# Kernel optimization log

Hardware: AMD Instinct MI355X
Metric: run time of the kernel (lower is better)

The kernel has to match this reference:

```python
import jax, jax.numpy as jnp
import numpy as np

D_MODEL, NHEAD, INT_DIM = 1024, 16, 4096
HEAD_DIM = D_MODEL // NHEAD
EPS = 1e-5


def _layernorm(x, gamma, beta):
    mu = jnp.mean(x, axis=-1, keepdims=True)
    var = jnp.var(x, axis=-1, keepdims=True)
    return (x - mu) * jax.lax.rsqrt(var + EPS) * gamma + beta


def setup_inputs() -> dict:
    key = jax.random.key(0)
    ks = jax.random.split(key, 16)
    B, T = 2, 2048
    s = 0.02
    inp = {
        'x': jax.random.normal(ks[0], (B, T, D_MODEL), dtype=jnp.float32),
        'Wq': jax.random.normal(ks[1], (D_MODEL, D_MODEL), dtype=jnp.float32) * s,
        'bq': jnp.zeros((D_MODEL,), jnp.float32),
        'Wk': jax.random.normal(ks[2], (D_MODEL, D_MODEL), dtype=jnp.float32) * s,
        'bk': jnp.zeros((D_MODEL,), jnp.float32),
        'Wv': jax.random.normal(ks[3], (D_MODEL, D_MODEL), dtype=jnp.float32) * s,
        'bv': jnp.zeros((D_MODEL,), jnp.float32),
        'Wo': jax.random.normal(ks[4], (D_MODEL, D_MODEL), dtype=jnp.float32) * s,
        'bo': jnp.zeros((D_MODEL,), jnp.float32),
        'ln1_g': jnp.ones((D_MODEL,), jnp.float32),
        'ln1_b': jnp.zeros((D_MODEL,), jnp.float32),
        'ln2_g': jnp.ones((D_MODEL,), jnp.float32),
        'ln2_b': jnp.zeros((D_MODEL,), jnp.float32),
        'W1': jax.random.normal(ks[5], (D_MODEL, INT_DIM), dtype=jnp.float32) * s,
        'b1': jnp.zeros((INT_DIM,), jnp.float32),
        'W2': jax.random.normal(ks[6], (INT_DIM, D_MODEL), dtype=jnp.float32) * s,
        'b2': jnp.zeros((D_MODEL,), jnp.float32),
    }
    return inp


def reference(x, Wq, bq, Wk, bk, Wv, bv, Wo, bo, ln1_g, ln1_b, ln2_g, ln2_b, W1, b1, W2, b2):
    B, T, D = x.shape
    # projections
    q = (x @ Wq + bq).reshape(B, T, NHEAD, HEAD_DIM).transpose(0, 2, 1, 3)
    k = (x @ Wk + bk).reshape(B, T, NHEAD, HEAD_DIM).transpose(0, 2, 1, 3)
    v = (x @ Wv + bv).reshape(B, T, NHEAD, HEAD_DIM).transpose(0, 2, 1, 3)
    # attention: [B,H,T,T] scores, softmax over keys
    scores = jnp.einsum('bhqd,bhkd->bhqk', q, k) / jnp.sqrt(jnp.float32(HEAD_DIM))
    attn = jax.nn.softmax(scores, axis=-1)
    out = jnp.einsum('bhqk,bhkd->bhqd', attn, v)
    out = out.transpose(0, 2, 1, 3).reshape(B, T, D)
    attn_output = out @ Wo + bo
    # residual + layernorm 1
    h = _layernorm(x + attn_output, ln1_g, ln1_b)
    # FFN
    ff = jax.nn.relu(h @ W1 + b1) @ W2 + b2
    # residual + layernorm 2
    return _layernorm(h + ff, ln2_g, ln2_b)
```

## Files before the change

### kernel.cpp

```cpp
#include <hip/hip_runtime.h>
#include <cstdint>

#define DEVI __device__ __forceinline__

typedef float f32x4 __attribute__((ext_vector_type(4)));
typedef __bf16 bf16x8 __attribute__((ext_vector_type(8)));
typedef unsigned int u32x4v __attribute__((ext_vector_type(4)));
typedef unsigned short u16;
typedef unsigned int u32;
typedef unsigned long long u64;

#define LOG2E 1.44269504088896f
#define QSCALE (0.125f * LOG2E)

DEVI u16 bf16bits(float f) {
    u32 u = __builtin_bit_cast(u32, f);
    u32 r = u + 0x7fffu + ((u >> 16) & 1u);
    return (u16)(r >> 16);
}

DEVI u32 pack2bf(float a, float b) {
    u16 x = __builtin_bit_cast(u16, (__bf16)a);
    u16 y = __builtin_bit_cast(u16, (__bf16)b);
    return (u32)x | ((u32)y << 16);
}

DEVI void gload16(const void* g, const void* l) {
    __builtin_amdgcn_global_load_lds(
        (const __attribute__((address_space(1))) void*)(u64)(uintptr_t)g,
        (__attribute__((address_space(3))) void*)(u32)(uintptr_t)l,
        16, 0, 0);
}

#define VMCNT0_BARRIER()                                   \
    asm volatile("s_waitcnt vmcnt(0)" ::: "memory");       \
    __builtin_amdgcn_s_barrier()

__global__ __launch_bounds__(256)
void prep_kernel(const float* __restrict__ x, u16* __restrict__ xb,
                 const float* __restrict__ Wq, const float* __restrict__ Wk,
                 const float* __restrict__ Wv, const float* __restrict__ Wo,
                 u16* __restrict__ Wqt, u16* __restrict__ Wkt,
                 u16* __restrict__ Wvt, u16* __restrict__ Wot,
                 const float* __restrict__ W1, u16* __restrict__ W1t,
                 const float* __restrict__ W2, u16* __restrict__ W2t) {
    __shared__ float t[64][65];
    const int b = blockIdx.x;
    const int tid = threadIdx.x;
    if (b < 4096) {
        int i = b * 256 + tid;
        float4 v = ((const float4*)x)[i];
        ((uint2*)xb)[i] = make_uint2(pack2bf(v.x, v.y), pack2bf(v.z, v.w));
        return;
    }
    const float* src;
    u16* dst;
    int K_, N_, k0, n0;
    if (b < 5120) {
        int l = b - 4096;
        int z = l >> 8;
        l &= 255;
        src = z == 0 ? Wq : z == 1 ? Wk : z == 2 ? Wv : Wo;
        dst = z == 0 ? Wqt : z == 1 ? Wkt : z == 2 ? Wvt : Wot;
        K_ = 1024; N_ = 1024;
        k0 = (l & 15) * 64; n0 = (l >> 4) * 64;
    } else if (b < 6144) {
        int l = b - 5120;
        src = W1; dst = W1t; K_ = 1024; N_ = 4096;
        k0 = (l & 15) * 64; n0 = (l >> 4) * 64;
    } else {
        int l = b - 6144;
        src = W2; dst = W2t; K_ = 4096; N_ = 1024;
        k0 = (l & 63) * 64; n0 = (l >> 6) * 64;
    }
#pragma unroll
    for (int i = 0; i < 16; i++) {
        int idx = i * 256 + tid;
        int r = idx >> 6, c = idx & 63;
        t[r][c] = src[(u64)(k0 + r) * N_ + n0 + c];
    }
    __syncthreads();
#pragma unroll
    for (int i = 0; i < 16; i++) {
        int idx = i * 256 + tid;
        int r = idx >> 6, c = idx & 63;
        dst[(u64)(n0 + r) * K_ + k0 + c] = bf16bits(t[c][r]);
    }
}

enum { MODE_QK = 0, MODE_VT = 1, MODE_RESID = 2, MODE_RELU = 3 };

DEVI void gemm_core(const u16* __restrict__ A, const u16* __restrict__ Bt, int K_,
                    u16 (*ldsA)[128 * 64], u16 (*ldsB)[128 * 64],
                    f32x4 (&acc)[4][4], int m0, int n0) {
    const int tid = threadIdx.x;
    const int lane = tid & 63;
    const int wid = tid >> 6;
    const int wr = wid >> 1, wc = wid & 1;
    const int l15 = lane & 15, l4 = lane >> 4;
    const int srow = tid >> 3;
    const int sc = (tid & 7) ^ (srow & 7);

    const u16* ap[4];
    const u16* bp[4];
#pragma unroll
    for (int i = 0; i < 4; i++) {
        ap[i] = A + (u64)(m0 + i * 32 + srow) * K_ + sc * 8;
        bp[i] = Bt + (u64)(n0 + i * 32 + srow) * K_ + sc * 8;
    }

    auto stage = [&](int buf) {
#pragma unroll
        for (int i = 0; i < 4; i++) {
            gload16(ap[i], (const char*)ldsA[buf] + (i * 256 + tid) * 16);
            ap[i] += 64;
        }
#pragma unroll
        for (int i = 0; i < 4; i++) {
            gload16(bp[i], (const char*)ldsB[buf] + (i * 256 + tid) * 16);
            bp[i] += 64;
        }
    };

    auto compute = [&](const u16* A_, const u16* B_) {
#pragma unroll
        for (int ks = 0; ks < 2; ks++) {
            bf16x8 af[4], bfr[4];
#pragma unroll
            for (int mi = 0; mi < 4; mi++) {
                int row = wr * 64 + mi * 16 + l15;
                af[mi] = *(const bf16x8*)((const char*)A_ + row * 128 +
                                          (((ks * 4 + l4) ^ (row & 7)) * 16));
            }
#pragma unroll
            for (int ni = 0; ni < 4; ni++) {
                int row = wc * 64 + ni * 16 + l15;
                bfr[ni] = *(const bf16x8*)((const char*)B_ + row * 128 +
                                           (((ks * 4 + l4) ^ (row & 7)) * 16));
            }
            __builtin_amdgcn_s_setprio(1);
#pragma unroll
            for (int mi = 0; mi < 4; mi++)
#pragma unroll
                for (int ni = 0; ni < 4; ni++)
                    acc[mi][ni] = __builtin_amdgcn_mfma_f32_16x16x32_bf16(
                        af[mi], bfr[ni], acc[mi][ni], 0, 0, 0);
            __builtin_amdgcn_s_setprio(0);
        }
    };

    const int nk = K_ >> 6;
    stage(0);
    VMCNT0_BARRIER();
    for (int t = 0; t < nk; t += 2) {
        if (t + 1 < nk) stage(1);
        compute(ldsA[0], ldsB[0]);
        VMCNT0_BARRIER();
        if (t + 2 < nk) stage(0);
        compute(ldsA[1], ldsB[1]);
        VMCNT0_BARRIER();
    }
}

template <int MODE>
DEVI void gemm_epilogue(f32x4 (&acc)[4][4], const float* __restrict__ bias,
                        const float* __restrict__ resid, void* __restrict__ outp,
                        int N_, int m0, int n0, float scale) {
    const int tid = threadIdx.x;
    const int lane = tid & 63;
    const int wid = tid >> 6;
    const int wr = wid >> 1, wc = wid & 1;
    const int l15 = lane & 15, l4 = lane >> 4;
#pragma unroll
    for (int mi = 0; mi < 4; mi++) {
#pragma unroll
        for (int ni = 0; ni < 4; ni++) {
            const int n = n0 + wc * 64 + ni * 16 + l15;
            const float bv = bias[n];
            const int mb = m0 + wr * 64 + mi * 16 + l4 * 4;
            if (MODE == MODE_VT) {
                const int b = mb >> 11, t = mb & 2047;
                const int hh = n >> 6, d = n & 63;
                u32 lo = pack2bf(acc[mi][ni][0] + bv, acc[mi][ni][1] + bv);
                u32 hi = pack2bf(acc[mi][ni][2] + bv, acc[mi][ni][3] + bv);
                u64 idx = ((u64)((b << 4) + hh) * 64 + d) * 2048 + t;
                *(uint2*)((u16*)outp + idx) = make_uint2(lo, hi);
            } else {
#pragma unroll
                for (int r = 0; r < 4; r++) {
                    const int m = mb + r;
                    const float v = acc[mi][ni][r] + bv;
                    if (MODE == MODE_QK) {
                        const int b = m >> 11, t = m & 2047;
                        const int hh = n >> 6, d = n & 63;
                        ((u16*)outp)[(((u64)((b << 4) + hh) * 2048 + t) << 6) + d] =
                            bf16bits(v * scale);
                    } else if (MODE == MODE_RESID) {
                        const u64 i2 = (u64)m * N_ + n;
                        ((float*)outp)[i2] = v + resid[i2];
                    } else {
                        ((u16*)outp)[(u64)m * N_ + n] = bf16bits(fmaxf(v, 0.f));
                    }
                }
            }
        }
    }
}

template <int MODE>
__global__ __launch_bounds__(256, 2)
void gemm_kernel(const u16* __restrict__ A, const u16* __restrict__ Bt,
                 const float* __restrict__ bias, const float* __restrict__ resid,
                 void* __restrict__ outp, int N_, int K_) {
    __shared__ u16 ldsA[2][128 * 64];
    __shared__ u16 ldsB[2][128 * 64];
    const int m0 = blockIdx.x * 128;
    const int n0 = blockIdx.y * 128;
    f32x4 acc[4][4];
#pragma unroll
    for (int i = 0; i < 4; i++)
#pragma unroll
        for (int j = 0; j < 4; j++) acc[i][j] = (f32x4){0.f, 0.f, 0.f, 0.f};
    gemm_core(A, Bt, K_, ldsA, ldsB, acc, m0, n0);
    gemm_epilogue<MODE>(acc, bias, resid, outp, N_, m0, n0, 1.f);
}

__global__ __launch_bounds__(256, 2)
void gemm_qkv_kernel(const u16* __restrict__ A,
                     const u16* __restrict__ Wq, const u16* __restrict__ Wk,
                     const u16* __restrict__ Wv,
                     const float* __restrict__ bq, const float* __restrict__ bk,
                     const float* __restrict__ bv,
                     u16* __restrict__ Qo, u16* __restrict__ Ko, u16* __restrict__ Vo) {
    __shared__ u16 ldsA[2][128 * 64];
    __shared__ u16 ldsB[2][128 * 64];
    const int z = blockIdx.z;
    const u16* Bt = z == 0 ? Wq : z == 1 ? Wk : Wv;
    const float* bias = z == 0 ? bq : z == 1 ? bk : bv;
    const int m0 = blockIdx.x * 128;
    const int n0 = blockIdx.y * 128;
    f32x4 acc[4][4];
#pragma unroll
    for (int i = 0; i < 4; i++)
#pragma unroll
        for (int j = 0; j < 4; j++) acc[i][j] = (f32x4){0.f, 0.f, 0.f, 0.f};
    gemm_core(A, Bt, 1024, ldsA, ldsB, acc, m0, n0);
    if (z == 2)
        gemm_epilogue<MODE_VT>(acc, bias, nullptr, Vo, 1024, m0, n0, 1.f);
    else
        gemm_epilogue<MODE_QK>(acc, bias, nullptr, z == 0 ? Qo : Ko, 1024, m0, n0,
                               z == 0 ? QSCALE : 1.f);
}

__global__ __launch_bounds__(256, 2)
void gemm_n64_kernel(const u16* __restrict__ A, const u16* __restrict__ Bt,
                     const float* __restrict__ bias, const float* __restrict__ resid,
                     float* __restrict__ outp, int K_) {
    __shared__ u16 ldsA[2][128 * 64];
    __shared__ u16 ldsB[2][64 * 64];
    const int tid = threadIdx.x;
    const int lane = tid & 63;
    const int wid = tid >> 6;
    const int m0 = blockIdx.x * 128;
    const int n0 = blockIdx.y * 64;
    const int l15 = lane & 15, l4 = lane >> 4;
    const int srow = tid >> 3;
    const int sc = (tid & 7) ^ (srow & 7);

    const u16* ap[4];
    const u16* bp[2];
#pragma unroll
    for (int i = 0; i < 4; i++)
        ap[i] = A + (u64)(m0 + i * 32 + srow) * K_ + sc * 8;
#pragma unroll
    for (int i = 0; i < 2; i++)
        bp[i] = Bt + (u64)(n0 + i * 32 + srow) * K_ + sc * 8;

    auto stage = [&](int buf) {
#pragma unroll
        for (int i = 0; i < 4; i++) {
            gload16(ap[i], (const char*)ldsA[buf] + (i * 256 + tid) * 16);
            ap[i] += 64;
        }
#pragma unroll
        for (int i = 0; i < 2; i++) {
            gload16(bp[i], (const char*)ldsB[buf] + (i * 256 + tid) * 16);
            bp[i] += 64;
        }
    };

    f32x4 acc[2][4];
#pragma unroll
    for (int i = 0; i < 2; i++)
#pragma unroll
        for (int j = 0; j < 4; j++) acc[i][j] = (f32x4){0.f, 0.f, 0.f, 0.f};

    auto compute = [&](const u16* A_, const u16* B_) {
#pragma unroll
        for (int ks = 0; ks < 2; ks++) {
            bf16x8 af[2], bfr[4];
#pragma unroll
            for (int mi = 0; mi < 2; mi++) {
                int row = wid * 32 + mi * 16 + l15;
                af[mi] = *(const bf16x8*)((const char*)A_ + row * 128 +
                                          (((ks * 4 + l4) ^ (row & 7)) * 16));
            }
#pragma unroll
            for (int ni = 0; ni < 4; ni++) {
                int row = ni * 16 + l15;
                bfr[ni] = *(const bf16x8*)((const char*)B_ + row * 128 +
                                           (((ks * 4 + l4) ^ (row & 7)) * 16));
            }
            __builtin_amdgcn_s_setprio(1);
#pragma unroll
            for (int mi = 0; mi < 2; mi++)
#pragma unroll
                for (int ni = 0; ni < 4; ni++)
                    acc[mi][ni] = __builtin_amdgcn_mfma_f32_16x16x32_bf16(
                        af[mi], bfr[ni], acc[mi][ni], 0, 0, 0);
            __builtin_amdgcn_s_setprio(0);
        }
    };

    const int nk = K_ >> 6;
    stage(0);
    VMCNT0_BARRIER();
    for (int t = 0; t < nk; t += 2) {
        if (t + 1 < nk) stage(1);
        compute(ldsA[0], ldsB[0]);
        VMCNT0_BARRIER();
        if (t + 2 < nk) stage(0);
        compute(ldsA[1], ldsB[1]);
        VMCNT0_BARRIER();
    }

#pragma unroll
    for (int mi = 0; mi < 2; mi++) {
#pragma unroll
        for (int ni = 0; ni < 4; ni++) {
            const int n = n0 + ni * 16 + l15;
            const float bv = bias[n];
            const int mb = m0 + wid * 32 + mi * 16 + l4 * 4;
#pragma unroll
            for (int r = 0; r < 4; r++) {
                const u64 i2 = (u64)(mb + r) * 1024 + n;
                outp[i2] = acc[mi][ni][r] + bv + resid[i2];
            }
        }
    }
}

__global__ __launch_bounds__(256, 5)
void attn_kernel(const u16* __restrict__ Qg, const u16* __restrict__ Kg,
                 const u16* __restrict__ Vtg, u16* __restrict__ Og) {
    __shared__ u16 ldsK[2][64 * 64];
    __shared__ u16 ldsV[2][64 * 64];
    const int tid = threadIdx.x;
    const int lane = tid & 63;
    const int w = tid >> 6;
    const int l15 = lane & 15, l4 = lane >> 4;
    const int id = blockIdx.x;
    const int swz = (id & 7) * 128 + (id >> 3);
    const int bh = swz >> 5;
    const int qblk = swz & 31;
    const u64 kvbase = (u64)bh * 2048 * 64;
    const int qw0 = qblk * 64 + w * 16;

    const int srow = tid >> 3;
    const int sc8 = ((tid & 7) ^ (srow & 7)) * 8;
    const u16* kq0 = Kg + kvbase + (u64)srow * 64 + sc8;
    const u16* kq1 = Kg + kvbase + (u64)(srow + 32) * 64 + sc8;
    const u16* vq0 = Vtg + kvbase + (u64)srow * 2048 + sc8;
    const u16* vq1 = Vtg + kvbase + (u64)(srow + 32) * 2048 + sc8;

    auto stage = [&](int buf) {
        gload16(kq0, (const char*)ldsK[buf] + tid * 16);
        gload16(kq1, (const char*)ldsK[buf] + (256 + tid) * 16);
        gload16(vq0, (const char*)ldsV[buf] + tid * 16);
        gload16(vq1, (const char*)ldsV[buf] + (256 + tid) * 16);
        kq0 += 4096; kq1 += 4096; vq0 += 64; vq1 += 64;
    };

    stage(0);

    bf16x8 aq[2];
#pragma unroll
    for (int ks = 0; ks < 2; ks++)
        aq[ks] = *(const bf16x8*)(Qg + kvbase + (u64)(qw0 + l15) * 64 + ks * 32 + l4 * 8);

    const u32x4v onesw = {0x3F803F80u, 0x3F803F80u, 0x3F803F80u, 0x3F803F80u};
    const bf16x8 aones = __builtin_bit_cast(bf16x8, onesw);

    f32x4 acco[4];
#pragma unroll
    for (int i = 0; i < 4; i++) acco[i] = (f32x4){0.f, 0.f, 0.f, 0.f};
    f32x4 lacc = (f32x4){0.f, 0.f, 0.f, 0.f};

    auto tile_body = [&](const u16* K_, const u16* V_) {
        f32x4 sf[4];
#pragma unroll
        for (int f = 0; f < 4; f++) sf[f] = (f32x4){0.f, 0.f, 0.f, 0.f};
#pragma unroll
        for (int ks = 0; ks < 2; ks++) {
            bf16x8 ak[4];
#pragma unroll
            for (int f = 0; f < 4; f++) {
                int row = f * 16 + l15;
                ak[f] = *(const bf16x8*)((const char*)K_ + row * 128 +
                                         (((ks * 4 + l4) ^ (row & 7)) * 16));
            }
            __builtin_amdgcn_s_setprio(1);
#pragma unroll
            for (int f = 0; f < 4; f++)
                sf[f] = __builtin_amdgcn_mfma_f32_16x16x32_bf16(ak[f], aq[ks], sf[f], 0, 0, 0);
            __builtin_amdgcn_s_setprio(0);
        }

        u32 A[4], B[4];
#pragma unroll
        for (int f = 0; f < 4; f++) {
            float p0 = exp2f(sf[f][0]);
            float p1 = exp2f(sf[f][1]);
            float p2 = exp2f(sf[f][2]);
            float p3 = exp2f(sf[f][3]);
            A[f] = pack2bf(p0, p1);
            B[f] = pack2bf(p2, p3);
        }
        asm volatile("v_permlane32_swap_b32 %0, %1" : "+v"(A[0]), "+v"(A[1]));
        asm volatile("v_permlane16_swap_b32 %0, %1" : "+v"(A[0]), "+v"(A[1]));
        asm volatile("v_permlane32_swap_b32 %0, %1" : "+v"(B[0]), "+v"(B[1]));
        asm volatile("v_permlane16_swap_b32 %0, %1" : "+v"(B[0]), "+v"(B[1]));
        asm volatile("v_permlane32_swap_b32 %0, %1" : "+v"(A[2]), "+v"(A[3]));
        asm volatile("v_permlane16_swap_b32 %0, %1" : "+v"(A[2]), "+v"(A[3]));
        asm volatile("v_permlane32_swap_b32 %0, %1" : "+v"(B[2]), "+v"(B[3]));
        asm volatile("v_permlane16_swap_b32 %0, %1" : "+v"(B[2]), "+v"(B[3]));

#pragma unroll
        for (int ks = 0; ks < 2; ks++) {
            u32x4v pw = {A[2 * ks], B[2 * ks], A[2 * ks + 1], B[2 * ks + 1]};
            bf16x8 pfrag = __builtin_bit_cast(bf16x8, pw);
            bf16x8 av[4];
#pragma unroll
            for (int nf = 0; nf < 4; nf++) {
                int row = nf * 16 + l15;
                av[nf] = *(const bf16x8*)((const char*)V_ + row * 128 +
                                          (((ks * 4 + l4) ^ (row & 7)) * 16));
            }
            __builtin_amdgcn_s_setprio(1);
            lacc = __builtin_amdgcn_mfma_f32_16x16x32_bf16(aones, pfrag, lacc, 0, 0, 0);
#pragma unroll
            for (int nf = 0; nf < 4; nf++)
                acco[nf] = __builtin_amdgcn_mfma_f32_16x16x32_bf16(av[nf], pfrag, acco[nf], 0, 0, 0);
            __builtin_amdgcn_s_setprio(0);
        }
    };

    VMCNT0_BARRIER();

    for (int t = 0; t < 32; t += 2) {
        if (t + 1 < 32) stage(1);
        tile_body(ldsK[0], ldsV[0]);
        VMCNT0_BARRIER();
        if (t + 2 < 32) stage(0);
        tile_body(ldsK[1], ldsV[1]);
        VMCNT0_BARRIER();
    }

    const float inv = 1.f / lacc[0];

    const int b = bh >> 4, h = bh & 15;
    const int tq = qw0 + l15;
#pragma unroll
    for (int nf = 0; nf < 4; nf++) {
        const int d = nf * 16 + l4 * 4;
        u32 lo = pack2bf(acco[nf][0] * inv, acco[nf][1] * inv);
        u32 hi = pack2bf(acco[nf][2] * inv, acco[nf][3] * inv);
        *(uint2*)(Og + ((u64)(b * 2048 + tq) << 10) + h * 64 + d) = make_uint2(lo, hi);
    }
}

template <bool WB16>
__global__ __launch_bounds__(256, 4)
void ln_kernel(const float* __restrict__ in, const float* __restrict__ gam,
               const float* __restrict__ bet, float* __restrict__ outf,
               u16* __restrict__ outb) {
    __shared__ float red[2][4];
    const int row = blockIdx.x;
    const int tid = threadIdx.x;
    float4 v = ((const float4*)(in + (u64)row * 1024))[tid];
    float s = v.x + v.y + v.z + v.w;
    float sq = v.x * v.x + v.y * v.y + v.z * v.z + v.w * v.w;
#pragma unroll
    for (int sh = 1; sh < 64; sh <<= 1) {
        s += __shfl_xor(s, sh, 64);
        sq += __shfl_xor(sq, sh, 64);
    }
    if ((tid & 63) == 0) { red[0][tid >> 6] = s; red[1][tid >> 6] = sq; }
    __syncthreads();
    s = red[0][0] + red[0][1] + red[0][2] + red[0][3];
    sq = red[1][0] + red[1][1] + red[1][2] + red[1][3];
    float mu = s * (1.f / 1024.f);
    float var = sq * (1.f / 1024.f) - mu * mu;
    float inv = rsqrtf(var + 1e-5f);
    float4 g = ((const float4*)gam)[tid];
    float4 bb = ((const float4*)bet)[tid];
    float4 o;
    o.x = (v.x - mu) * inv * g.x + bb.x;
    o.y = (v.y - mu) * inv * g.y + bb.y;
    o.z = (v.z - mu) * inv * g.z + bb.z;
    o.w = (v.w - mu) * inv * g.w + bb.w;
    ((float4*)(outf + (u64)row * 1024))[tid] = o;
    if (WB16) {
        ((uint2*)(outb + (u64)row * 1024))[tid] = make_uint2(pack2bf(o.x, o.y), pack2bf(o.z, o.w));
    }
}

extern "C" void kernel_launch(void* const* d_in, const int* in_sizes, int n_in,
                              void* d_out, int out_size, void* d_ws, size_t ws_size,
                              hipStream_t stream) {
    (void)in_sizes; (void)n_in; (void)out_size; (void)ws_size;
    const float* x  = (const float*)d_in[0];
    const float* Wq = (const float*)d_in[1];
    const float* bq = (const float*)d_in[2];
    const float* Wk = (const float*)d_in[3];
    const float* bk = (const float*)d_in[4];
    const float* Wv = (const float*)d_in[5];
    const float* bv = (const float*)d_in[6];
    const float* Wo = (const float*)d_in[7];
    const float* bo = (const float*)d_in[8];
    const float* g1 = (const float*)d_in[9];
    const float* be1 = (const float*)d_in[10];
    const float* g2 = (const float*)d_in[11];
    const float* be2 = (const float*)d_in[12];
    const float* W1 = (const float*)d_in[13];
    const float* b1 = (const float*)d_in[14];
    const float* W2 = (const float*)d_in[15];
    const float* b2 = (const float*)d_in[16];

    char* ws = (char*)d_ws;
    const u64 MB = 1024ull * 1024ull;
    u16* xb    = (u16*)(ws + 0);
    u16* Wqt   = (u16*)(ws + 8 * MB);
    u16* Wkt   = (u16*)(ws + 10 * MB);
    u16* Wvt   = (u16*)(ws + 12 * MB);
    u16* Wot   = (u16*)(ws + 14 * MB);
    u16* W1t   = (u16*)(ws + 16 * MB);
    u16* W2t   = (u16*)(ws + 24 * MB);
    u16* Qb    = (u16*)(ws + 32 * MB);
    u16* Kb    = (u16*)(ws + 40 * MB);
    u16* Vtb   = (u16*)(ws + 48 * MB);
    u16* Ob    = (u16*)(ws + 56 * MB);
    float* pre1 = (float*)(ws + 64 * MB);
    float* hf  = (float*)(ws + 80 * MB);
    u16* hb    = (u16*)(ws + 96 * MB);
    u16* ffb   = (u16*)(ws + 104 * MB);
    float* pre2 = (float*)(ws + 64 * MB);

    prep_kernel<<<7168, 256, 0, stream>>>(x, xb, Wq, Wk, Wv, Wo,
                                          Wqt, Wkt, Wvt, Wot, W1, W1t, W2, W2t);

    gemm_qkv_kernel<<<dim3(32, 8, 3), 256, 0, stream>>>(xb, Wqt, Wkt, Wvt,
                                                        bq, bk, bv, Qb, Kb, Vtb);

    attn_kernel<<<1024, 256, 0, stream>>>(Qb, Kb, Vtb, Ob);

    gemm_n64_kernel<<<dim3(32, 16), 256, 0, stream>>>(Ob, Wot, bo, x, pre1, 1024);
    ln_kernel<true><<<4096, 256, 0, stream>>>(pre1, g1, be1, hf, hb);
    gemm_kernel<MODE_RELU><<<dim3(32, 32), 256, 0, stream>>>(hb, W1t, b1, nullptr, ffb, 4096, 1024);
    gemm_n64_kernel<<<dim3(32, 16), 256, 0, stream>>>(ffb, W2t, b2, hf, pre2, 4096);
    ln_kernel<false><<<4096, 256, 0, stream>>>(pre2, g2, be2, (float*)d_out, nullptr);
}
```

Measured before the change: 211.8 us.

## Split attention KV range in two with fp32 partials and combine kernel

Each attention block now processes only half of the key/value sequence, doubling the grid to 2048 blocks. Each block writes unnormalized fp32 partial outputs and row sums. A new combine kernel adds the two partials, normalizes them and packs the result to bf16. The aim is more concurrent blocks per CU for better latency hiding. In exchange it adds an extra launch plus about 64MB of fp32 partial traffic. The plain sum-combine is only correct if the kernel uses a fixed softmax offset rather than a running max.

Result: slower. 220.1 us (+3.9%).

```diff
diff --git a/kernel.cpp b/kernel.cpp
--- a/kernel.cpp
+++ b/kernel.cpp
@@ -352,7 +352,8 @@
 
 __global__ __launch_bounds__(256, 5)
 void attn_kernel(const u16* __restrict__ Qg, const u16* __restrict__ Kg,
-                 const u16* __restrict__ Vtg, u16* __restrict__ Og) {
+                 const u16* __restrict__ Vtg, float* __restrict__ Of,
+                 float* __restrict__ Lf) {
     __shared__ u16 ldsK[2][64 * 64];
     __shared__ u16 ldsV[2][64 * 64];
     const int tid = threadIdx.x;
@@ -360,18 +361,21 @@
     const int w = tid >> 6;
     const int l15 = lane & 15, l4 = lane >> 4;
     const int id = blockIdx.x;
-    const int swz = (id & 7) * 128 + (id >> 3);
-    const int bh = swz >> 5;
-    const int qblk = swz & 31;
+    const int swz = (id & 7) * 256 + (id >> 3);
+    const int bh = swz >> 6;
+    const int rem = swz & 63;
+    const int qblk = rem >> 1;
+    const int split = rem & 1;
     const u64 kvbase = (u64)bh * 2048 * 64;
     const int qw0 = qblk * 64 + w * 16;
+    const int kbase = split * 1024;
 
     const int srow = tid >> 3;
     const int sc8 = ((tid & 7) ^ (srow & 7)) * 8;
-    const u16* kq0 = Kg + kvbase + (u64)srow * 64 + sc8;
-    const u16* kq1 = Kg + kvbase + (u64)(srow + 32) * 64 + sc8;
-    const u16* vq0 = Vtg + kvbase + (u64)srow * 2048 + sc8;
-    const u16* vq1 = Vtg + kvbase + (u64)(srow + 32) * 2048 + sc8;
+    const u16* kq0 = Kg + kvbase + (u64)(kbase + srow) * 64 + sc8;
+    const u16* kq1 = Kg + kvbase + (u64)(kbase + srow + 32) * 64 + sc8;
+    const u16* vq0 = Vtg + kvbase + (u64)srow * 2048 + kbase + sc8;
+    const u16* vq1 = Vtg + kvbase + (u64)(srow + 32) * 2048 + kbase + sc8;
 
     auto stage = [&](int buf) {
         gload16(kq0, (const char*)ldsK[buf] + tid * 16);
@@ -457,26 +461,42 @@
 
     VMCNT0_BARRIER();
 
-    for (int t = 0; t < 32; t += 2) {
-        if (t + 1 < 32) stage(1);
+    for (int t = 0; t < 16; t += 2) {
+        if (t + 1 < 16) stage(1);
         tile_body(ldsK[0], ldsV[0]);
         VMCNT0_BARRIER();
-        if (t + 2 < 32) stage(0);
+        if (t + 2 < 16) stage(0);
         tile_body(ldsK[1], ldsV[1]);
         VMCNT0_BARRIER();
     }
 
-    const float inv = 1.f / lacc[0];
-
     const int b = bh >> 4, h = bh & 15;
     const int tq = qw0 + l15;
+    float* of = Of + (u64)split * (4096ull * 1024ull);
 #pragma unroll
     for (int nf = 0; nf < 4; nf++) {
         const int d = nf * 16 + l4 * 4;
-        u32 lo = pack2bf(acco[nf][0] * inv, acco[nf][1] * inv);
-        u32 hi = pack2bf(acco[nf][2] * inv, acco[nf][3] * inv);
-        *(uint2*)(Og + ((u64)(b * 2048 + tq) << 10) + h * 64 + d) = make_uint2(lo, hi);
-    }
+        *(f32x4*)(of + (((u64)(b * 2048 + tq)) << 10) + h * 64 + d) = acco[nf];
+    }
+    if (l4 == 0) Lf[split * 65536 + (bh << 11) + tq] = lacc[0];
+}
+
+__global__ __launch_bounds__(256)
+void attn_combine_kernel(const float* __restrict__ Of, const float* __restrict__ Lf,
+                         u16* __restrict__ Og) {
+    const int e4 = blockIdx.x * 256 + threadIdx.x;
+    const u64 e = (u64)e4 * 4;
+    const int m = (int)(e >> 10);
+    const int c = (int)(e & 1023);
+    const int h = c >> 6;
+    const int b = m >> 11, t = m & 2047;
+    const int lidx = ((b * 16 + h) << 11) + t;
+    const float inv = 1.f / (Lf[lidx] + Lf[65536 + lidx]);
+    float4 a0 = ((const float4*)Of)[e4];
+    float4 a1 = ((const float4*)(Of + 4096ull * 1024ull))[e4];
+    u32 lo = pack2bf((a0.x + a1.x) * inv, (a0.y + a1.y) * inv);
+    u32 hi = pack2bf((a0.z + a1.z) * inv, (a0.w + a1.w) * inv);
+    ((uint2*)Og)[e4] = make_uint2(lo, hi);
 }
 
 template <bool WB16>
@@ -550,6 +570,8 @@
     u16* Kb    = (u16*)(ws + 40 * MB);
     u16* Vtb   = (u16*)(ws + 48 * MB);
     u16* Ob    = (u16*)(ws + 56 * MB);
+    float* Of  = (float*)(ws + 64 * MB);
+    float* Lf  = (float*)(ws + 96 * MB);
     float* pre1 = (float*)(ws + 64 * MB);
     float* hf  = (float*)(ws + 80 * MB);
     u16* hb    = (u16*)(ws + 96 * MB);
@@ -562,7 +584,8 @@
     gemm_qkv_kernel<<<dim3(32, 8, 3), 256, 0, stream>>>(xb, Wqt, Wkt, Wvt,
                                                         bq, bk, bv, Qb, Kb, Vtb);
 
-    attn_kernel<<<1024, 256, 0, stream>>>(Qb, Kb, Vtb, Ob);
+    attn_kernel<<<2048, 256, 0, stream>>>(Qb, Kb, Vtb, Of, Lf);
+    attn_combine_kernel<<<4096, 256, 0, stream>>>(Of, Lf, Ob);
 
     gemm_n64_kernel<<<dim3(32, 16), 256, 0, stream>>>(Ob, Wot, bo, x, pre1, 1024);
     ln_kernel<true><<<4096, 256, 0, stream>>>(pre1, g1, be1, hf, hb);
```

## Triple-buffer K/V tiles in attention with partial vmcnt waits and raw exp

Applied to the files above, without the earlier changes.

The attention kernel moves from double-buffered K/V staging to a three-slot ring of LDS buffers. Two tiles are prefetched up front, and each iteration waits only until the older tile's loads land (vmcnt(4)), so one tile's loads stay in flight while the current tile is computed. This lets each iteration wait on the oldest outstanding tile instead of draining all loads. The change also replaces exp2f with a direct v_exp_f32 instruction to drop the library's range handling. The larger LDS footprint goes with lowering the launch-bounds occupancy hint from 5 to 3 blocks, which may reduce latency hiding across blocks.

Measured after the change: 204.5 us. 1.04x faster.

```diff
diff --git a/kernel.cpp b/kernel.cpp
--- a/kernel.cpp
+++ b/kernel.cpp
@@ -23,6 +23,12 @@
     u16 x = __builtin_bit_cast(u16, (__bf16)a);
     u16 y = __builtin_bit_cast(u16, (__bf16)b);
     return (u32)x | ((u32)y << 16);
+}
+
+DEVI float ex2(float x) {
+    float r;
+    asm("v_exp_f32 %0, %1" : "=v"(r) : "v"(x));
+    return r;
 }
 
 DEVI void gload16(const void* g, const void* l) {
@@ -350,11 +356,11 @@
     }
 }
 
-__global__ __launch_bounds__(256, 5)
+__global__ __launch_bounds__(256, 3)
 void attn_kernel(const u16* __restrict__ Qg, const u16* __restrict__ Kg,
                  const u16* __restrict__ Vtg, u16* __restrict__ Og) {
-    __shared__ u16 ldsK[2][64 * 64];
-    __shared__ u16 ldsV[2][64 * 64];
+    __shared__ u16 ldsK[3][64 * 64];
+    __shared__ u16 ldsV[3][64 * 64];
     const int tid = threadIdx.x;
     const int lane = tid & 63;
     const int w = tid >> 6;
@@ -381,12 +387,14 @@
         kq0 += 4096; kq1 += 4096; vq0 += 64; vq1 += 64;
     };
 
-    stage(0);
-
     bf16x8 aq[2];
 #pragma unroll
     for (int ks = 0; ks < 2; ks++)
         aq[ks] = *(const bf16x8*)(Qg + kvbase + (u64)(qw0 + l15) * 64 + ks * 32 + l4 * 8);
+    asm volatile("s_waitcnt vmcnt(0)" ::: "memory");
+
+    stage(0);
+    stage(1);
 
     const u32x4v onesw = {0x3F803F80u, 0x3F803F80u, 0x3F803F80u, 0x3F803F80u};
     const bf16x8 aones = __builtin_bit_cast(bf16x8, onesw);
@@ -419,10 +427,10 @@
         u32 A[4], B[4];
 #pragma unroll
         for (int f = 0; f < 4; f++) {
-            float p0 = exp2f(sf[f][0]);
-            float p1 = exp2f(sf[f][1]);
-            float p2 = exp2f(sf[f][2]);
-            float p3 = exp2f(sf[f][3]);
+            float p0 = ex2(sf[f][0]);
+            float p1 = ex2(sf[f][1]);
+            float p2 = ex2(sf[f][2]);
+            float p3 = ex2(sf[f][3]);
             A[f] = pack2bf(p0, p1);
             B[f] = pack2bf(p2, p3);
         }
@@ -455,16 +463,19 @@
         }
     };
 
-    VMCNT0_BARRIER();
-
-    for (int t = 0; t < 32; t += 2) {
-        if (t + 1 < 32) stage(1);
-        tile_body(ldsK[0], ldsV[0]);
-        VMCNT0_BARRIER();
-        if (t + 2 < 32) stage(0);
-        tile_body(ldsK[1], ldsV[1]);
-        VMCNT0_BARRIER();
-    }
+    int cb = 0;
+    int sb = 2;
+    for (int t = 0; t < 31; t++) {
+        asm volatile("s_waitcnt vmcnt(4)" ::: "memory");
+        __builtin_amdgcn_s_barrier();
+        if (t < 30) stage(sb);
+        tile_body(ldsK[cb], ldsV[cb]);
+        cb = (cb == 2) ? 0 : cb + 1;
+        sb = (sb == 2) ? 0 : sb + 1;
+    }
+    asm volatile("s_waitcnt vmcnt(0)" ::: "memory");
+    __builtin_amdgcn_s_barrier();
+    tile_body(ldsK[cb], ldsV[cb]);
 
     const float inv = 1.f / lacc[0];
 
```
